# Optimization experiments

Measured on AMD Instinct MI355X. Metric: run time of the kernel, lower is better.

Reference implementation:

```python
import jax, jax.numpy as jnp
import numpy as np

INPUT_SIZE = 100
HIDDEN_SIZE = 200
OUTPUT_SIZE = 1


def setup_inputs() -> dict:
    key = jax.random.key(0)
    k0, k1, k2, k3, k4, k5, k6 = jax.random.split(key, 7)
    s = 1.0 / np.sqrt(HIDDEN_SIZE)  # torch RNNCell/Linear init scale
    inp = jax.random.normal(k0, (128, 1024, INPUT_SIZE), dtype=jnp.float32)
    W_ih = jax.random.uniform(k1, (HIDDEN_SIZE, INPUT_SIZE), minval=-s, maxval=s)
    W_hh = jax.random.uniform(k2, (HIDDEN_SIZE, HIDDEN_SIZE), minval=-s, maxval=s)
    b_ih = jax.random.uniform(k3, (HIDDEN_SIZE,), minval=-s, maxval=s)
    b_hh = jax.random.uniform(k4, (HIDDEN_SIZE,), minval=-s, maxval=s)
    W_out = jax.random.uniform(k5, (OUTPUT_SIZE, HIDDEN_SIZE), minval=-s, maxval=s)
    b_out = jax.random.uniform(k6, (OUTPUT_SIZE,), minval=-s, maxval=s)
    return {"input": inp, "W_ih": W_ih, "W_hh": W_hh, "b_ih": b_ih,
            "b_hh": b_hh, "W_out": W_out, "b_out": b_out}


def reference(input, W_ih, W_hh, b_ih, b_hh, W_out, b_out):
    B, T, _ = input.shape
    # Precompute input projections for all timesteps in one GEMM: [B,T,H]
    x_proj = jnp.einsum('bti,hi->bth', input, W_ih) + b_ih + b_hh

    def step(h, xp_t):  # h: [B,H], xp_t: [B,H]
        h = jax.nn.relu(xp_t + h @ W_hh.T)
        o = h @ W_out.T + b_out  # identity output nonlinearity (out_nlin='linear')
        return h, (h, o)

    h0 = jnp.zeros((B, HIDDEN_SIZE), dtype=input.dtype)
    _, (hiddens, outputs) = jax.lax.scan(step, h0, jnp.swapaxes(x_proj, 0, 1))
    outputs = jnp.swapaxes(outputs, 0, 1)  # [B,T,O]
    hiddens = jnp.swapaxes(hiddens, 0, 1)  # [B,T,H] (torch returns list of [B,H])
    return (outputs, hiddens)
```

## Files before the change

kernel.cpp:

```cpp
#include <hip/hip_runtime.h>

#define BB 128
#define TT 1024
#define II 100
#define HH 200

__global__ __launch_bounds__(256, 1) void rnn_xproj(
    const float* __restrict__ x, const float* __restrict__ Wih,
    const float* __restrict__ bih, const float* __restrict__ bhh,
    float* __restrict__ hid)
{
    __shared__ __align__(16) float xs[128 * II];
    const int tid = threadIdx.x;
    const int j = tid;
    const int jl = (j < HH) ? j : (HH - 1);

    float w[II];
    const float4* wrow = (const float4*)(Wih + jl * II);
#pragma unroll
    for (int kk = 0; kk < II / 4; ++kk) {
        float4 v = wrow[kk];
        w[4 * kk + 0] = v.x; w[4 * kk + 1] = v.y;
        w[4 * kk + 2] = v.z; w[4 * kk + 3] = v.w;
    }
    const float bias = bih[jl] + bhh[jl];

    const long long r0 = (long long)blockIdx.x * 128;
    const float4* src = (const float4*)(x + r0 * II);
    float4* dst = (float4*)xs;
    for (int p = tid; p < 128 * II / 4; p += 256) dst[p] = src[p];
    __syncthreads();

    for (int row = 0; row < 128; ++row) {
        float acc0 = 0.f, acc1 = 0.f, acc2 = 0.f, acc3 = 0.f;
        const float4* xr = (const float4*)(xs + row * II);
#pragma unroll
        for (int kk = 0; kk < II / 4; ++kk) {
            float4 v = xr[kk];
            acc0 += w[4 * kk + 0] * v.x; acc1 += w[4 * kk + 1] * v.y;
            acc2 += w[4 * kk + 2] * v.z; acc3 += w[4 * kk + 3] * v.w;
        }
        if (j < HH)
            hid[(r0 + row) * HH + j] = bias + ((acc0 + acc1) + (acc2 + acc3));
    }
}

__global__ __launch_bounds__(256, 1) void rnn_recur(
    const float* __restrict__ Whh, float* __restrict__ hid)
{
    __shared__ __align__(16) float hbuf[2][HH + 8];
    const int tid = threadIdx.x;
    const int j = tid;
    const int jl = (j < HH) ? j : (HH - 1);

    float w[HH];
    const float4* wrow = (const float4*)(Whh + jl * HH);
#pragma unroll
    for (int kk = 0; kk < HH / 4; ++kk) {
        float4 v = wrow[kk];
        w[4 * kk + 0] = v.x; w[4 * kk + 1] = v.y;
        w[4 * kk + 2] = v.z; w[4 * kk + 3] = v.w;
    }

    if (tid < HH) { hbuf[0][tid] = 0.f; }
    __syncthreads();

    float* rowp = hid + (long long)blockIdx.x * TT * HH;
    int cur = 0;
    for (int t = 0; t < TT; ++t) {
        float xpv = (j < HH) ? rowp[j] : 0.f;
        float acc0 = 0.f, acc1 = 0.f, acc2 = 0.f, acc3 = 0.f;
        const float4* hr = (const float4*)hbuf[cur];
#pragma unroll
        for (int kk = 0; kk < HH / 4; ++kk) {
            float4 v = hr[kk];
            acc0 += w[4 * kk + 0] * v.x; acc1 += w[4 * kk + 1] * v.y;
            acc2 += w[4 * kk + 2] * v.z; acc3 += w[4 * kk + 3] * v.w;
        }
        float hv = fmaxf(xpv + ((acc0 + acc1) + (acc2 + acc3)), 0.f);
        if (j < HH) { rowp[j] = hv; hbuf[cur ^ 1][j] = hv; }
        __syncthreads();
        cur ^= 1;
        rowp += HH;
    }
}

__global__ __launch_bounds__(256) void rnn_out(
    const float* __restrict__ hid, const float* __restrict__ Wout,
    const float* __restrict__ bout, float* __restrict__ out)
{
    const int wave = threadIdx.x >> 6;
    const int lane = threadIdx.x & 63;
    const long long r = (long long)blockIdx.x * 4 + wave;
    const float* hr = hid + r * HH;
    float p = 0.f;
#pragma unroll
    for (int m = 0; m < 4; ++m) {
        int idx = lane + 64 * m;
        if (idx < HH) p += Wout[idx] * hr[idx];
    }
#pragma unroll
    for (int off = 32; off; off >>= 1) p += __shfl_down(p, off, 64);
    if (lane == 0) out[r] = p + bout[0];
}

extern "C" void kernel_launch(void* const* d_in, const int* in_sizes, int n_in,
                              void* d_out, int out_size, void* d_ws, size_t ws_size,
                              hipStream_t stream)
{
    const float* x    = (const float*)d_in[0];
    const float* Wih  = (const float*)d_in[1];
    const float* Whh  = (const float*)d_in[2];
    const float* bih  = (const float*)d_in[3];
    const float* bhh  = (const float*)d_in[4];
    const float* Wout = (const float*)d_in[5];
    const float* bout = (const float*)d_in[6];

    float* out = (float*)d_out;
    float* hid = out + (long long)BB * TT;

    rnn_xproj<<<(BB * TT) / 128, 256, 0, stream>>>(x, Wih, bih, bhh, hid);
    rnn_recur<<<BB, 256, 0, stream>>>(Whh, hid);
    rnn_out<<<(BB * TT) / 4, 256, 0, stream>>>(hid, Wout, bout, out);
}
```

Baseline: 969.1 us.

## Split recurrent dot products across thread pairs and prefetch input projections

The recurrent kernel now uses 512 threads, with two threads per hidden unit. Each thread covers half of the 200-wide dot product and the two halves are combined with a shuffle, which shortens the serial latency of every timestep. The next timestep's input projection is loaded ahead of time to hide global memory latency, and register pressure per thread drops. The output kernel now has each block handle 64 rows and loads W_out into registers once, cutting the block count; it adds a shuffle per step and a larger block that has to synchronise.

Result: slower. 1.069 ms (+10.3%).

```diff
diff --git a/kernel.cpp b/kernel.cpp
--- a/kernel.cpp
+++ b/kernel.cpp
@@ -45,43 +45,50 @@
     }
 }
 
-__global__ __launch_bounds__(256, 1) void rnn_recur(
+__global__ __launch_bounds__(512, 2) void rnn_recur(
     const float* __restrict__ Whh, float* __restrict__ hid)
 {
-    __shared__ __align__(16) float hbuf[2][HH + 8];
-    const int tid = threadIdx.x;
-    const int j = tid;
-    const int jl = (j < HH) ? j : (HH - 1);
+    __shared__ __align__(16) float hbuf[2][208];
+    const int tid  = threadIdx.x;
+    const int half = tid & 1;
+    const int j    = tid >> 1;
+    const bool act = (j < HH);
+    const int  jl  = act ? j : (HH - 1);
 
-    float w[HH];
-    const float4* wrow = (const float4*)(Whh + jl * HH);
+    float4 w[25];
+    const float4* wrow = (const float4*)(Whh + jl * HH + 100 * half);
 #pragma unroll
-    for (int kk = 0; kk < HH / 4; ++kk) {
-        float4 v = wrow[kk];
-        w[4 * kk + 0] = v.x; w[4 * kk + 1] = v.y;
-        w[4 * kk + 2] = v.z; w[4 * kk + 3] = v.w;
-    }
+    for (int kk = 0; kk < 25; ++kk) w[kk] = wrow[kk];
 
-    if (tid < HH) { hbuf[0][tid] = 0.f; }
+    if (tid < HH) hbuf[0][tid] = 0.f;
     __syncthreads();
 
     float* rowp = hid + (long long)blockIdx.x * TT * HH;
+    float xpv = (act && half == 0) ? rowp[j] : 0.f;
     int cur = 0;
+
     for (int t = 0; t < TT; ++t) {
-        float xpv = (j < HH) ? rowp[j] : 0.f;
-        float acc0 = 0.f, acc1 = 0.f, acc2 = 0.f, acc3 = 0.f;
-        const float4* hr = (const float4*)hbuf[cur];
+        float xpn = 0.f;
+        if (act && half == 0 && t + 1 < TT) xpn = rowp[HH + j];
+
+        const float4* hr = (const float4*)(hbuf[cur] + 100 * half);
+        float a0 = 0.f, a1 = 0.f, a2 = 0.f, a3 = 0.f;
 #pragma unroll
-        for (int kk = 0; kk < HH / 4; ++kk) {
+        for (int kk = 0; kk < 25; ++kk) {
             float4 v = hr[kk];
-            acc0 += w[4 * kk + 0] * v.x; acc1 += w[4 * kk + 1] * v.y;
-            acc2 += w[4 * kk + 2] * v.z; acc3 += w[4 * kk + 3] * v.w;
+            a0 += w[kk].x * v.x; a1 += w[kk].y * v.y;
+            a2 += w[kk].z * v.z; a3 += w[kk].w * v.w;
         }
-        float hv = fmaxf(xpv + ((acc0 + acc1) + (acc2 + acc3)), 0.f);
-        if (j < HH) { rowp[j] = hv; hbuf[cur ^ 1][j] = hv; }
+        float p = (a0 + a1) + (a2 + a3);
+        p += __shfl_xor(p, 1, 64);
+
+        if (act && half == 0) {
+            float hv = fmaxf(xpv + p, 0.f);
+            rowp[j] = hv;
+            hbuf[cur ^ 1][j] = hv;
+        }
         __syncthreads();
-        cur ^= 1;
-        rowp += HH;
+        cur ^= 1; xpv = xpn; rowp += HH;
     }
 }
 
@@ -91,17 +98,29 @@
 {
     const int wave = threadIdx.x >> 6;
     const int lane = threadIdx.x & 63;
-    const long long r = (long long)blockIdx.x * 4 + wave;
-    const float* hr = hid + r * HH;
-    float p = 0.f;
+
+    float wv[4];
 #pragma unroll
     for (int m = 0; m < 4; ++m) {
         int idx = lane + 64 * m;
-        if (idx < HH) p += Wout[idx] * hr[idx];
+        wv[m] = (idx < HH) ? Wout[idx] : 0.f;
     }
+    const float bo = bout[0];
+
+    const long long rbase = (long long)blockIdx.x * 64;
+#pragma unroll 1
+    for (int rr = wave; rr < 64; rr += 4) {
+        const float* hr = hid + (rbase + rr) * HH;
+        float p = 0.f;
 #pragma unroll
-    for (int off = 32; off; off >>= 1) p += __shfl_down(p, off, 64);
-    if (lane == 0) out[r] = p + bout[0];
+        for (int m = 0; m < 4; ++m) {
+            int idx = lane + 64 * m;
+            if (idx < HH) p += wv[m] * hr[idx];
+        }
+#pragma unroll
+        for (int off = 32; off; off >>= 1) p += __shfl_down(p, off, 64);
+        if (lane == 0) out[rbase + rr] = p + bo;
+    }
 }
 
 extern "C" void kernel_launch(void* const* d_in, const int* in_sizes, int n_in,
@@ -120,6 +139,6 @@
     float* hid = out + (long long)BB * TT;
 
     rnn_xproj<<<(BB * TT) / 128, 256, 0, stream>>>(x, Wih, bih, bhh, hid);
-    rnn_recur<<<BB, 256, 0, stream>>>(Whh, hid);
-    rnn_out<<<(BB * TT) / 4, 256, 0, stream>>>(hid, Wout, bout, out);
+    rnn_recur<<<BB, 512, 0, stream>>>(Whh, hid);
+    rnn_out<<<(BB * TT) / 64, 256, 0, stream>>>(hid, Wout, bout, out);
 }
```
